# Optimization experiments

Measured on AMD Instinct MI355X. Metric: run time of the kernel, lower is better.

Reference implementation:

```python
import jax, jax.numpy as jnp
import numpy as np

N = 10000
E = 160000
IN_CH, HID, OUT = 14, 128, 4
HEADS = 8
NEG_SLOPE = 0.2


def setup_inputs() -> dict:
    key = jax.random.key(0)
    ks = jax.random.split(key, 16)
    glorot = lambda k, shape: jax.random.normal(k, shape, jnp.float32) * np.sqrt(2.0 / (shape[0] + shape[-1]))
    inp = {
        'x': jax.random.normal(ks[0], (N, IN_CH), jnp.float32),
        'edge_index': jax.random.randint(ks[1], (2, E), 0, N, jnp.int64),
        # layer 1: 14 -> 8 heads x 128, concat
        'W1': glorot(ks[2], (IN_CH, HEADS * HID)),
        'a_src1': glorot(ks[3], (HEADS, HID)),
        'a_dst1': glorot(ks[4], (HEADS, HID)),
        'b1': jnp.zeros((HEADS * HID,), jnp.float32),
        # layer 2: 1024 -> 8 heads x 128, concat
        'W2': glorot(ks[5], (HEADS * HID, HEADS * HID)),
        'a_src2': glorot(ks[6], (HEADS, HID)),
        'a_dst2': glorot(ks[7], (HEADS, HID)),
        'b2': jnp.zeros((HEADS * HID,), jnp.float32),
        # layer 3: 1024 -> 1 head x 4, mean (concat=False)
        'W3': glorot(ks[8], (HEADS * HID, OUT)),
        'a_src3': glorot(ks[9], (1, OUT)),
        'a_dst3': glorot(ks[10], (1, OUT)),
        'b3': jnp.zeros((OUT,), jnp.float32),
    }
    return inp


def gat_conv(x, src, dst, W, a_src, a_dst, b, heads, out_ch, concat):
    n = x.shape[0]
    h = (x @ W).reshape(n, heads, out_ch)                      # [N,H,C]
    al_s = jnp.sum(h * a_src, axis=-1)                         # [N,H]
    al_d = jnp.sum(h * a_dst, axis=-1)                         # [N,H]
    e = al_s[src] + al_d[dst]                                  # [E,H]
    e = jnp.where(e > 0, e, NEG_SLOPE * e)                     # LeakyReLU(0.2)
    # segment softmax over incoming edges of each dst node
    m = jax.ops.segment_max(e, dst, num_segments=n)
    ex = jnp.exp(e - m[dst])
    z = jax.ops.segment_sum(ex, dst, num_segments=n)
    alpha = ex / (z[dst] + 1e-16)                              # [E,H]
    out = jax.ops.segment_sum(h[src] * alpha[:, :, None], dst, num_segments=n)  # [N,H,C]
    out = out.reshape(n, heads * out_ch) if concat else out.mean(axis=1)
    return out + b


def reference(x, edge_index, W1, a_src1, a_dst1, b1, W2, a_src2, a_dst2, b2, W3, a_src3, a_dst3, b3):
    n = x.shape[0]
    # add self-loops (PyG GATConv default)
    loop = jnp.arange(n, dtype=edge_index.dtype)
    src = jnp.concatenate([edge_index[0], loop])
    dst = jnp.concatenate([edge_index[1], loop])
    # dropout layers are identity in eval mode
    h = gat_conv(x, src, dst, W1, a_src1, a_dst1, b1, HEADS, HID, True)
    h = jax.nn.relu(h)
    h = gat_conv(h, src, dst, W2, a_src2, a_dst2, b2, HEADS, HID, True)
    h = jax.nn.relu(h)
    h = gat_conv(h, src, dst, W3, a_src3, a_dst3, b3, 1, OUT, False)
    h = jax.nn.relu(h)
    return h
```

## Files before the change

### kernel.cpp

```cpp
#include <hip/hip_runtime.h>

typedef unsigned short ushort_t;
typedef unsigned int uint32;

#define N_NODES 10000
#define N_EDGES 160000
#define ET (N_NODES + N_EDGES)
#define MPAD 10112
#define HT 1024
#define HEADS 8
#define NEG 0.2f

#define O_FLAG     0
#define O_SRC      256
#define O_DST      (O_SRC + 680192)
#define O_COUNTS   (O_DST + 680192)
#define O_OFFS     (O_COUNTS + 40192)
#define O_CURS     (O_OFFS + 40192)
#define O_SSORT    (O_CURS + 40192)
#define O_ALS      (O_SSORT + 680192)
#define O_ALD      (O_ALS + 320000)
#define O_AL3S     (O_ALD + 320000)
#define O_AL3D     (O_AL3S + 40192)
#define O_H3       (O_AL3D + 40192)
#define O_XF       (O_H3 + 160000)
#define O_W1F      (O_XF + 560128)
#define O_AS1F     (O_W1F + 57344)
#define O_W3F      (O_AS1F + 24576)
#define O_S3F      (O_W3F + 16384)
#define O_W2T      (O_S3F + 768)
#define O_BUFA     (O_W2T + 2097152)
#define O_BUFB     (O_BUFA + 20709376)

__device__ __forceinline__ float bf2f(ushort_t u){ return __uint_as_float(((uint32)u) << 16); }
__device__ __forceinline__ ushort_t f2bf(float f){
    uint32 x = __float_as_uint(f);
    return (ushort_t)((x + 0x7fffu + ((x >> 16) & 1u)) >> 16);
}
__device__ __forceinline__ void unpack2(uint32 u, float& lo, float& hi){
    lo = __uint_as_float(u << 16);
    hi = __uint_as_float(u & 0xffff0000u);
}

typedef __bf16 bf16x8 __attribute__((ext_vector_type(8)));
typedef float  f32x4  __attribute__((ext_vector_type(4)));

typedef const __attribute__((address_space(1))) uint32* gas1_u32;
typedef       __attribute__((address_space(3))) uint32* las3_u32;

__device__ __forceinline__ void gload_lds16(const void* g, void* l){
    __builtin_amdgcn_global_load_lds((gas1_u32)g, (las3_u32)l, 16, 0, 0);
}

__device__ __forceinline__ int probe_f32(const uint32* __restrict__ w){
    int cnt = 0;
    for (int i = 0; i < 256; i++){
        uint32 e = (w[i] >> 7) & 0xffu;
        cnt += (e >= 64u && e <= 160u) ? 1 : 0;
    }
    return (cnt > 200) ? 0 : 1;
}
__device__ __forceinline__ int probe_edge64(const int* __restrict__ ei){
    int nz = 0;
    for (int i = 0; i < 128; i++) nz |= ei[2*i + 1];
    return (nz == 0) ? 1 : 0;
}

struct CvtArgs {
    const void* src[12];
    float*      dst[12];
    int         n[12];
};

__global__ __launch_bounds__(256) void k_setup(CvtArgs a, const void* __restrict__ W2,
                                               const uint32* __restrict__ w1raw,
                                               const int* __restrict__ eiraw,
                                               int* __restrict__ counts,
                                               ushort_t* __restrict__ W2T,
                                               int* __restrict__ flags){
    __shared__ ushort_t tile[32][33];
    int slice = blockIdx.y;
    int tid = threadIdx.x;
    if (slice < 12){
        int n = a.n[slice];
        int base = blockIdx.x * 1024 + tid * 4;
        if (base >= n) return;
        int f32 = probe_f32(w1raw);
        const void* s = a.src[slice];
        float* d = a.dst[slice];
        #pragma unroll
        for (int j = 0; j < 4; j++){
            int i = base + j;
            if (i < n) d[i] = f32 ? ((const float*)s)[i] : bf2f(((const ushort_t*)s)[i]);
        }
    } else if (slice == 12){
        if (blockIdx.x == 10){
            if (tid == 0) flags[0] = probe_edge64(eiraw);
            if (tid == 1) flags[1] = probe_f32(w1raw);
            return;
        }
        if (blockIdx.x < 10){
            int i0 = blockIdx.x * 1024 + tid * 4;
            if (i0 + 3 < N_NODES){
                *(int4*)(counts + i0) = make_int4(0,0,0,0);
            } else {
                for (int j = 0; j < 4; j++) if (i0 + j < N_NODES) counts[i0 + j] = 0;
            }
        }
    } else {
        int f32 = probe_f32(w1raw);
        int bx = blockIdx.x & 31, by = blockIdx.x >> 5;
        int cx = tid & 31;
        int ry = (tid >> 5) * 4;
        #pragma unroll
        for (int r = 0; r < 4; r++){
            size_t idx = (size_t)(by*32 + ry + r)*1024 + bx*32 + cx;
            tile[ry + r][cx] = f32 ? f2bf(((const float*)W2)[idx]) : ((const ushort_t*)W2)[idx];
        }
        __syncthreads();
        #pragma unroll
        for (int r = 0; r < 4; r++)
            W2T[(size_t)(bx*32 + ry + r)*1024 + by*32 + cx] = tile[cx][ry + r];
    }
}

__global__ __launch_bounds__(256) void k_extract_hist(const void* __restrict__ ei, const int* __restrict__ flags,
                                                      int* __restrict__ src, int* __restrict__ dst,
                                                      int* __restrict__ counts){
    int i = blockIdx.x * 256 + threadIdx.x;
    int is64 = flags[0];
    int s = -1, d = -1;
    if (i < N_EDGES){
        if (is64){
            const long long* p = (const long long*)ei;
            s = (int)p[i]; d = (int)p[N_EDGES + i];
        } else {
            const int* p = (const int*)ei;
            s = p[i]; d = p[N_EDGES + i];
        }
    } else if (i < ET){
        s = i - N_EDGES; d = s;
    }
    if (d >= 0){
        src[i] = s; dst[i] = d;
        atomicAdd(&counts[d], 1);
    }
}

__global__ __launch_bounds__(1024) void k_scan(const int* __restrict__ counts, int* __restrict__ offs,
                                               int* __restrict__ cursors, int n){
    __shared__ int wsum[16];
    __shared__ int running_s;
    int tid = threadIdx.x;
    int lane = tid & 63, wid = tid >> 6;
    if (tid == 0) running_s = 0;
    __syncthreads();
    for (int base = 0; base < n; base += 1024){
        int i = base + tid;
        int v = (i < n) ? counts[i] : 0;
        int x = v;
        #pragma unroll
        for (int d = 1; d < 64; d <<= 1){
            int t = __shfl_up(x, d, 64);
            if (lane >= d) x += t;
        }
        if (lane == 63) wsum[wid] = x;
        __syncthreads();
        if (wid == 0 && lane < 16){
            int w = wsum[lane];
            #pragma unroll
            for (int d = 1; d < 16; d <<= 1){
                int t = __shfl_up(w, d, 64);
                if (lane >= d) w += t;
            }
            wsum[lane] = w;
        }
        __syncthreads();
        int wprefix = (wid == 0) ? 0 : wsum[wid - 1];
        int run = running_s;
        int excl = run + wprefix + (x - v);
        if (i < n){ offs[i] = excl; cursors[i] = excl; }
        __syncthreads();
        if (tid == 0) running_s = run + wsum[15];
        __syncthreads();
    }
    if (tid == 0) offs[n] = running_s;
}

__global__ __launch_bounds__(256) void k_scatter(const int* __restrict__ src, const int* __restrict__ dst,
                                                 int* __restrict__ cursors, int* __restrict__ ssort){
    int i = blockIdx.x * 256 + threadIdx.x;
    if (i < ET){
        int pos = atomicAdd(&cursors[dst[i]], 1);
        ssort[pos] = src[i];
    }
}

__global__ __launch_bounds__(256) void k_gemm1f(const float* __restrict__ x, const float* __restrict__ W1,
                                                const float* __restrict__ a_src, const float* __restrict__ a_dst,
                                                ushort_t* __restrict__ h1,
                                                float* __restrict__ alS, float* __restrict__ alD){
    __shared__ float w1s[14 * HT];
    int tid = threadIdx.x;
    for (int i = tid * 4; i < 14 * HT; i += 1024)
        *(float4*)(w1s + i) = *(const float4*)(W1 + i);
    int c0 = tid * 4;
    float4 sv = *(const float4*)(a_src + c0);
    float4 dv = *(const float4*)(a_dst + c0);
    int head = tid >> 5, l32 = tid & 31;
    __syncthreads();
    for (int n = blockIdx.x; n < N_NODES; n += gridDim.x){
        float a0=0.f, a1=0.f, a2=0.f, a3=0.f;
        #pragma unroll
        for (int k = 0; k < 14; k++){
            float xv = x[n*14 + k];
            float4 w = *(const float4*)(w1s + k*HT + c0);
            a0 += xv*w.x; a1 += xv*w.y; a2 += xv*w.z; a3 += xv*w.w;
        }
        uint2 o;
        o.x = (uint32)f2bf(a0) | ((uint32)f2bf(a1) << 16);
        o.y = (uint32)f2bf(a2) | ((uint32)f2bf(a3) << 16);
        *(uint2*)(h1 + (size_t)n*HT + c0) = o;
        float h0,h1v,h2,h3v;
        unpack2(o.x, h0, h1v); unpack2(o.y, h2, h3v);
        float s = h0*sv.x + h1v*sv.y + h2*sv.z + h3v*sv.w;
        float d = h0*dv.x + h1v*dv.y + h2*dv.z + h3v*dv.w;
        #pragma unroll
        for (int of = 16; of; of >>= 1){ s += __shfl_xor(s, of, 32); d += __shfl_xor(d, of, 32); }
        if (l32 == 0){ alS[n*HEADS + head] = s; alD[n*HEADS + head] = d; }
    }
}

__global__ __launch_bounds__(256) void k_gat_agg(const ushort_t* __restrict__ H, const float* __restrict__ alS,
                                                 const float* __restrict__ alD, const int* __restrict__ offs,
                                                 const int* __restrict__ srcs, const float* __restrict__ bias,
                                                 ushort_t* __restrict__ out){
    int tid = threadIdx.x;
    int wv = tid >> 6, lane = tid & 63;
    int n = blockIdx.x * 2 + (wv >> 1);
    int half = wv & 1;
    int beg = offs[n], end = offs[n+1];
    int head = half*4 + (lane >> 4);
    float ad = alD[n*HEADS + head];

    int ch0 = half*512 + lane*8;
    const ushort_t* Hc = H + ch0;
    float m = -1e30f, z = 0.f;
    float c0=0.f,c1=0.f,c2=0.f,c3=0.f,c4=0.f,c5=0.f,c6=0.f,c7=0.f;
    for (int c = beg; c < end; c += 64){
        int cn = min(64, end - c);
        int sreg = (lane < cn) ? srcs[c + lane] : 0;
        int j = 0;
        for (; j + 4 <= cn; j += 4){
            int s0 = __shfl(sreg, j, 64);
            int s1 = __shfl(sreg, j+1, 64);
            int s2 = __shfl(sreg, j+2, 64);
            int s3 = __shfl(sreg, j+3, 64);
            uint4 u0 = *(const uint4*)(Hc + (size_t)s0*HT);
            uint4 u1 = *(const uint4*)(Hc + (size_t)s1*HT);
            uint4 u2 = *(const uint4*)(Hc + (size_t)s2*HT);
            uint4 u3 = *(const uint4*)(Hc + (size_t)s3*HT);
            float e0 = alS[s0*HEADS + head];
            float e1 = alS[s1*HEADS + head];
            float e2 = alS[s2*HEADS + head];
            float e3 = alS[s3*HEADS + head];
            float v0 = e0 + ad; v0 = v0 > 0.f ? v0 : NEG*v0;
            float v1 = e1 + ad; v1 = v1 > 0.f ? v1 : NEG*v1;
            float v2 = e2 + ad; v2 = v2 > 0.f ? v2 : NEG*v2;
            float v3 = e3 + ad; v3 = v3 > 0.f ? v3 : NEG*v3;
            float vm = fmaxf(fmaxf(v0, v1), fmaxf(v2, v3));
            if (vm > m){
                float sc = __expf(m - vm);
                z *= sc;
                c0*=sc; c1*=sc; c2*=sc; c3*=sc;
                c4*=sc; c5*=sc; c6*=sc; c7*=sc;
                m = vm;
            }
            float w0 = __expf(v0 - m);
            float w1 = __expf(v1 - m);
            float w2 = __expf(v2 - m);
            float w3 = __expf(v3 - m);
            z += (w0 + w1) + (w2 + w3);
            float f0,f1,f2,f3,f4,f5,f6,f7;
            unpack2(u0.x,f0,f1); unpack2(u0.y,f2,f3); unpack2(u0.z,f4,f5); unpack2(u0.w,f6,f7);
            c0+=w0*f0; c1+=w0*f1; c2+=w0*f2; c3+=w0*f3;
            c4+=w0*f4; c5+=w0*f5; c6+=w0*f6; c7+=w0*f7;
            unpack2(u1.x,f0,f1); unpack2(u1.y,f2,f3); unpack2(u1.z,f4,f5); unpack2(u1.w,f6,f7);
            c0+=w1*f0; c1+=w1*f1; c2+=w1*f2; c3+=w1*f3;
            c4+=w1*f4; c5+=w1*f5; c6+=w1*f6; c7+=w1*f7;
            unpack2(u2.x,f0,f1); unpack2(u2.y,f2,f3); unpack2(u2.z,f4,f5); unpack2(u2.w,f6,f7);
            c0+=w2*f0; c1+=w2*f1; c2+=w2*f2; c3+=w2*f3;
            c4+=w2*f4; c5+=w2*f5; c6+=w2*f6; c7+=w2*f7;
            unpack2(u3.x,f0,f1); unpack2(u3.y,f2,f3); unpack2(u3.z,f4,f5); unpack2(u3.w,f6,f7);
            c0+=w3*f0; c1+=w3*f1; c2+=w3*f2; c3+=w3*f3;
            c4+=w3*f4; c5+=w3*f5; c6+=w3*f6; c7+=w3*f7;
        }
        for (; j < cn; j++){
            int s0 = __shfl(sreg, j, 64);
            uint4 u0 = *(const uint4*)(Hc + (size_t)s0*HT);
            float v0 = alS[s0*HEADS + head] + ad;
            v0 = v0 > 0.f ? v0 : NEG*v0;
            if (v0 > m){
                float sc = __expf(m - v0);
                z *= sc;
                c0*=sc; c1*=sc; c2*=sc; c3*=sc;
                c4*=sc; c5*=sc; c6*=sc; c7*=sc;
                m = v0;
            }
            float w0 = __expf(v0 - m);
            z += w0;
            float f0,f1,f2,f3,f4,f5,f6,f7;
            unpack2(u0.x,f0,f1); unpack2(u0.y,f2,f3); unpack2(u0.z,f4,f5); unpack2(u0.w,f6,f7);
            c0+=w0*f0; c1+=w0*f1; c2+=w0*f2; c3+=w0*f3;
            c4+=w0*f4; c5+=w0*f5; c6+=w0*f6; c7+=w0*f7;
        }
    }
    float inv = 1.f / (z + 1e-16f);
    float4 b0 = *(const float4*)(bias + ch0);
    float4 b1 = *(const float4*)(bias + ch0 + 4);
    c0 = fmaxf(c0*inv+b0.x, 0.f); c1 = fmaxf(c1*inv+b0.y, 0.f);
    c2 = fmaxf(c2*inv+b0.z, 0.f); c3 = fmaxf(c3*inv+b0.w, 0.f);
    c4 = fmaxf(c4*inv+b1.x, 0.f); c5 = fmaxf(c5*inv+b1.y, 0.f);
    c6 = fmaxf(c6*inv+b1.z, 0.f); c7 = fmaxf(c7*inv+b1.w, 0.f);
    uint4 o;
    o.x = (uint32)f2bf(c0) | ((uint32)f2bf(c1) << 16);
    o.y = (uint32)f2bf(c2) | ((uint32)f2bf(c3) << 16);
    o.z = (uint32)f2bf(c4) | ((uint32)f2bf(c5) << 16);
    o.w = (uint32)f2bf(c6) | ((uint32)f2bf(c7) << 16);
    *(uint4*)(out + (size_t)n*HT + ch0) = o;
}

__global__ __launch_bounds__(256) void k_gemm2(const ushort_t* __restrict__ A, const ushort_t* __restrict__ BT,
                                               ushort_t* __restrict__ C,
                                               const float* __restrict__ aS, const float* __restrict__ aD,
                                               float* __restrict__ alS, float* __restrict__ alD){
    __shared__ ushort_t lbuf[2][2][128*64];
    float (*reds)[64][2] = (float (*)[64][2])lbuf;
    int L = blockIdx.x;
    int xcd = L & 7;
    int wi  = L >> 3;
    int bm  = xcd * 10 + (wi >> 3);
    int bn  = wi & 7;
    if (bm >= 79) return;
    int tid = threadIdx.x;
    int lane = tid & 63;
    int wave = tid >> 6;
    int wm = (wave & 1) * 64, wn = (wave >> 1) * 64;
    int lm = lane & 15, kg = lane >> 4;
    int c0 = (kg ^ (lm & 7)) * 8;
    f32x4 acc[4][4];
    #pragma unroll
    for (int i = 0; i < 4; i++)
        #pragma unroll
        for (int j = 0; j < 4; j++) acc[i][j] = (f32x4)0.0f;

    const int K = 1024;
    int rowA0 = bm * 128, rowB0 = bn * 128;

    auto stage = [&](int buf, int k0){
        #pragma unroll
        for (int it = 0; it < 4; ++it){
            int s = tid + it*256;
            int r = s >> 3;
            int q = (s & 7) ^ (r & 7);
            gload_lds16(A  + (size_t)(rowA0 + r)*K + k0 + q*8, &lbuf[buf][0][s*8]);
            gload_lds16(BT + (size_t)(rowB0 + r)*K + k0 + q*8, &lbuf[buf][1][s*8]);
        }
    };

    stage(0, 0);
    asm volatile("s_waitcnt vmcnt(0)" ::: "memory");
    __syncthreads();
    int cur = 0;
    for (int k0 = 0; k0 < K; k0 += 64){
        if (k0 + 64 < K) stage(cur ^ 1, k0 + 64);
        bf16x8 a0[4], a1[4], b0[4], b1[4];
        #pragma unroll
        for (int mt = 0; mt < 4; mt++){
            const ushort_t* base = &lbuf[cur][0][(wm + mt*16 + lm)*64];
            a0[mt] = *(const bf16x8*)(base + c0);
            a1[mt] = *(const bf16x8*)(base + (c0 ^ 32));
        }
        #pragma unroll
        for (int nt = 0; nt < 4; nt++){
            const ushort_t* base = &lbuf[cur][1][(wn + nt*16 + lm)*64];
            b0[nt] = *(const bf16x8*)(base + c0);
            b1[nt] = *(const bf16x8*)(base + (c0 ^ 32));
        }
        #pragma unroll
        for (int mt = 0; mt < 4; mt++)
            #pragma unroll
            for (int nt = 0; nt < 4; nt++)
                acc[mt][nt] = __builtin_amdgcn_mfma_f32_16x16x32_bf16(a0[mt], b0[nt], acc[mt][nt], 0, 0, 0);
        #pragma unroll
        for (int mt = 0; mt < 4; mt++)
            #pragma unroll
            for (int nt = 0; nt < 4; nt++)
                acc[mt][nt] = __builtin_amdgcn_mfma_f32_16x16x32_bf16(a1[mt], b1[nt], acc[mt][nt], 0, 0, 0);
        asm volatile("s_waitcnt vmcnt(0)" ::: "memory");
        __syncthreads();
        cur ^= 1;
    }
    #pragma unroll
    for (int mt = 0; mt < 4; mt++){
        int row_base = bm*128 + wm + mt*16 + kg*4;
        #pragma unroll
        for (int nt = 0; nt < 4; nt++){
            int col = bn*128 + wn + nt*16 + lm;
            #pragma unroll
            for (int r = 0; r < 4; r++){
                int row = row_base + r;
                if (row < N_NODES) C[(size_t)row*HT + col] = f2bf(acc[mt][nt][r]);
            }
        }
    }
    float as_l[4], ad_l[4];
    #pragma unroll
    for (int nt = 0; nt < 4; nt++){
        as_l[nt] = aS[bn*128 + wn + nt*16 + lm];
        ad_l[nt] = aD[bn*128 + wn + nt*16 + lm];
    }
    float psA[4][4], pdA[4][4];
    #pragma unroll
    for (int mt = 0; mt < 4; mt++){
        #pragma unroll
        for (int r = 0; r < 4; r++){
            float ps = acc[mt][0][r]*as_l[0] + acc[mt][1][r]*as_l[1]
                     + acc[mt][2][r]*as_l[2] + acc[mt][3][r]*as_l[3];
            float pd = acc[mt][0][r]*ad_l[0] + acc[mt][1][r]*ad_l[1]
                     + acc[mt][2][r]*ad_l[2] + acc[mt][3][r]*ad_l[3];
            #pragma unroll
            for (int o = 1; o < 16; o <<= 1){ ps += __shfl_xor(ps, o, 64); pd += __shfl_xor(pd, o, 64); }
            psA[mt][r] = ps; pdA[mt][r] = pd;
            if (wn == 64 && lm == 0){
                int rl = mt*16 + kg*4 + r;
                reds[wm >> 6][rl][0] = ps;
                reds[wm >> 6][rl][1] = pd;
            }
        }
    }
    __syncthreads();
    if (wn == 0 && lm == 0){
        #pragma unroll
        for (int mt = 0; mt < 4; mt++){
            #pragma unroll
            for (int r = 0; r < 4; r++){
                int rl = mt*16 + kg*4 + r;
                int row = bm*128 + wm + rl;
                if (row < N_NODES){
                    alS[row*HEADS + bn] = psA[mt][r] + reds[wm >> 6][rl][0];
                    alD[row*HEADS + bn] = pdA[mt][r] + reds[wm >> 6][rl][1];
                }
            }
        }
    }
}

__global__ __launch_bounds__(256) void k_gemm3(const ushort_t* __restrict__ A, const float* __restrict__ W3,
                                               const float* __restrict__ s3,
                                               float* __restrict__ h3, float* __restrict__ al3s, float* __restrict__ al3d){
    int tid = threadIdx.x;
    int lane = tid & 63, wave = tid >> 6;
    int n = blockIdx.x * 4 + wave;
    if (n >= N_NODES) return;
    float4 w3r[16];
    #pragma unroll
    for (int j = 0; j < 16; j++) w3r[j] = ((const float4*)W3)[lane*16 + j];
    const uint4* ap = (const uint4*)(A + (size_t)n*HT + lane*16);
    uint4 u0 = ap[0], u1 = ap[1];
    uint32 uu[8] = {u0.x,u0.y,u0.z,u0.w,u1.x,u1.y,u1.z,u1.w};
    float acc0=0.f, acc1=0.f, acc2=0.f, acc3=0.f;
    #pragma unroll
    for (int p = 0; p < 8; p++){
        float lo, hi;
        unpack2(uu[p], lo, hi);
        float4 wl = w3r[p*2], wh = w3r[p*2+1];
        acc0 += lo*wl.x + hi*wh.x;
        acc1 += lo*wl.y + hi*wh.y;
        acc2 += lo*wl.z + hi*wh.z;
        acc3 += lo*wl.w + hi*wh.w;
    }
    #pragma unroll
    for (int o = 32; o; o >>= 1){
        acc0 += __shfl_xor(acc0, o, 64); acc1 += __shfl_xor(acc1, o, 64);
        acc2 += __shfl_xor(acc2, o, 64); acc3 += __shfl_xor(acc3, o, 64);
    }
    if (lane == 0){
        *(float4*)(h3 + n*4) = make_float4(acc0, acc1, acc2, acc3);
        al3s[n] = acc0*s3[0] + acc1*s3[1] + acc2*s3[2] + acc3*s3[3];
        al3d[n] = acc0*s3[16] + acc1*s3[17] + acc2*s3[18] + acc3*s3[19];
    }
}

__global__ __launch_bounds__(256) void k_gat_agg3(const float* __restrict__ h3, const float* __restrict__ al3s,
                                                  const float* __restrict__ al3d, const int* __restrict__ offs,
                                                  const int* __restrict__ srcs, const float* __restrict__ b3,
                                                  const int* __restrict__ flags, void* __restrict__ out){
    int tid = threadIdx.x;
    int l = tid & 63, wave = tid >> 6;
    int n = blockIdx.x * 4 + wave;
    if (n >= N_NODES) return;
    int beg = offs[n], end = offs[n+1];
    float ad = al3d[n];
    float m = -1e30f;
    for (int e = beg + l; e < end; e += 64){
        float v = al3s[srcs[e]] + ad; v = v > 0.f ? v : NEG*v;
        m = fmaxf(m, v);
    }
    #pragma unroll
    for (int o = 32; o; o >>= 1) m = fmaxf(m, __shfl_xor(m, o, 64));
    float z = 0.f;
    for (int e = beg + l; e < end; e += 64){
        float v = al3s[srcs[e]] + ad; v = v > 0.f ? v : NEG*v;
        z += __expf(v - m);
    }
    #pragma unroll
    for (int o = 32; o; o >>= 1) z += __shfl_xor(z, o, 64);
    float inv = 1.f / (z + 1e-16f);
    float a0=0.f, a1=0.f, a2=0.f, a3=0.f;
    for (int e = beg + l; e < end; e += 64){
        int s = srcs[e];
        float v = al3s[s] + ad; v = v > 0.f ? v : NEG*v;
        float w = __expf(v - m) * inv;
        float4 hv = *(const float4*)(h3 + s*4);
        a0 += w*hv.x; a1 += w*hv.y; a2 += w*hv.z; a3 += w*hv.w;
    }
    #pragma unroll
    for (int o = 32; o; o >>= 1){
        a0 += __shfl_xor(a0, o, 64); a1 += __shfl_xor(a1, o, 64);
        a2 += __shfl_xor(a2, o, 64); a3 += __shfl_xor(a3, o, 64);
    }
    if (l == 0){
        float r0 = fmaxf(a0 + b3[0], 0.f);
        float r1 = fmaxf(a1 + b3[1], 0.f);
        float r2 = fmaxf(a2 + b3[2], 0.f);
        float r3 = fmaxf(a3 + b3[3], 0.f);
        if (flags[1]){
            float* o4 = (float*)out;
            o4[n*4+0]=r0; o4[n*4+1]=r1; o4[n*4+2]=r2; o4[n*4+3]=r3;
        } else {
            ushort_t* o2 = (ushort_t*)out;
            o2[n*4+0]=f2bf(r0); o2[n*4+1]=f2bf(r1); o2[n*4+2]=f2bf(r2); o2[n*4+3]=f2bf(r3);
        }
    }
}

extern "C" void kernel_launch(void* const* d_in, const int* in_sizes, int n_in,
                              void* d_out, int out_size, void* d_ws, size_t ws_size,
                              hipStream_t stream){
    const void* x   = d_in[0];
    const void* ei  = d_in[1];
    const void* W1  = d_in[2];
    const void* as1 = d_in[3];
    const void* ad1 = d_in[4];
    const void* b1  = d_in[5];
    const void* W2  = d_in[6];
    const void* as2 = d_in[7];
    const void* ad2 = d_in[8];
    const void* b2  = d_in[9];
    const void* W3  = d_in[10];
    const void* as3 = d_in[11];
    const void* ad3 = d_in[12];
    const void* b3  = d_in[13];

    char* ws = (char*)d_ws;
    int* flags     = (int*)(ws + O_FLAG);
    int* srcA      = (int*)(ws + O_SRC);
    int* dstA      = (int*)(ws + O_DST);
    int* counts    = (int*)(ws + O_COUNTS);
    int* offs      = (int*)(ws + O_OFFS);
    int* cursors   = (int*)(ws + O_CURS);
    int* ssort     = (int*)(ws + O_SSORT);
    float* alS     = (float*)(ws + O_ALS);
    float* alD     = (float*)(ws + O_ALD);
    float* al3s    = (float*)(ws + O_AL3S);
    float* al3d    = (float*)(ws + O_AL3D);
    float* h3      = (float*)(ws + O_H3);
    float* xF      = (float*)(ws + O_XF);
    float* W1F     = (float*)(ws + O_W1F);
    float* wvecF   = (float*)(ws + O_AS1F);
    float* W3F     = (float*)(ws + O_W3F);
    float* s3F     = (float*)(ws + O_S3F);
    ushort_t* W2T  = (ushort_t*)(ws + O_W2T);
    ushort_t* bufA = (ushort_t*)(ws + O_BUFA);
    ushort_t* bufB = (ushort_t*)(ws + O_BUFB);

    const int EB = (ET + 255) / 256;

    CvtArgs ca;
    ca.src[0]=x;   ca.dst[0]=xF;            ca.n[0]=140000;
    ca.src[1]=W1;  ca.dst[1]=W1F;           ca.n[1]=14336;
    ca.src[2]=as1; ca.dst[2]=wvecF+0*1024;  ca.n[2]=1024;
    ca.src[3]=ad1; ca.dst[3]=wvecF+1*1024;  ca.n[3]=1024;
    ca.src[4]=b1;  ca.dst[4]=wvecF+2*1024;  ca.n[4]=1024;
    ca.src[5]=as2; ca.dst[5]=wvecF+3*1024;  ca.n[5]=1024;
    ca.src[6]=ad2; ca.dst[6]=wvecF+4*1024;  ca.n[6]=1024;
    ca.src[7]=b2;  ca.dst[7]=wvecF+5*1024;  ca.n[7]=1024;
    ca.src[8]=W3;  ca.dst[8]=W3F;           ca.n[8]=4096;
    ca.src[9]=as3; ca.dst[9]=s3F+0;         ca.n[9]=4;
    ca.src[10]=ad3; ca.dst[10]=s3F+16;      ca.n[10]=4;
    ca.src[11]=b3;  ca.dst[11]=s3F+32;      ca.n[11]=4;

    k_setup<<<dim3(1024, 14), 256, 0, stream>>>(ca, W2, (const uint32*)W1, (const int*)ei,
                                                counts, W2T, flags);
    k_extract_hist<<<EB, 256, 0, stream>>>(ei, flags, srcA, dstA, counts);
    k_scan<<<1, 1024, 0, stream>>>(counts, offs, cursors, N_NODES);
    k_scatter<<<EB, 256, 0, stream>>>(srcA, dstA, cursors, ssort);

    k_gemm1f<<<512, 256, 0, stream>>>(xF, W1F, wvecF+0*1024, wvecF+1*1024, bufA, alS, alD);
    k_gat_agg<<<5000, 256, 0, stream>>>(bufA, alS, alD, offs, ssort, wvecF+2*1024, bufB);

    k_gemm2<<<640, 256, 0, stream>>>(bufB, W2T, bufA, wvecF+3*1024, wvecF+4*1024, alS, alD);
    k_gat_agg<<<5000, 256, 0, stream>>>(bufA, alS, alD, offs, ssort, wvecF+5*1024, bufB);

    k_gemm3<<<2500, 256, 0, stream>>>(bufB, W3F, s3F, h3, al3s, al3d);
    k_gat_agg3<<<2500, 256, 0, stream>>>(h3, al3s, al3d, offs, ssort, s3F+32, flags, d_out);
}
```

Measured before the change: 318.2 us.

## Restructure GAT aggregation: one wave per node-head, edge-parallel lane groups

The aggregation kernel now assigns each wave a single (node, head) pair. The four 16-lane groups in the wave process different edges in parallel, and their online-softmax partial states are merged at the end with cross-lane shuffles. The grid grows from 5000 to 20000 blocks, with the head index in the low block bits so neighbouring blocks share a node's source rows. The branchy max update is replaced by branchless FMA rescaling, and the output is written with a nontemporal store. This raises memory-level parallelism per node, but adds shuffle-reduction work and reads offsets and source lists once per head instead of once per node.

```diff
diff --git a/kernel.cpp b/kernel.cpp
--- a/kernel.cpp
+++ b/kernel.cpp
@@ -44,6 +44,7 @@
 
 typedef __bf16 bf16x8 __attribute__((ext_vector_type(8)));
 typedef float  f32x4  __attribute__((ext_vector_type(4)));
+typedef uint32 u32x4  __attribute__((ext_vector_type(4)));
 
 typedef const __attribute__((address_space(1))) uint32* gas1_u32;
 typedef       __attribute__((address_space(3))) uint32* las3_u32;
@@ -237,97 +238,104 @@
                                                  ushort_t* __restrict__ out){
     int tid = threadIdx.x;
     int wv = tid >> 6, lane = tid & 63;
-    int n = blockIdx.x * 2 + (wv >> 1);
-    int half = wv & 1;
+    int head = blockIdx.x & 7;
+    int n = (blockIdx.x >> 3) * 4 + wv;
+    if (n >= N_NODES) return;
     int beg = offs[n], end = offs[n+1];
-    int head = half*4 + (lane >> 4);
+    int g = lane >> 4;
+    int q = lane & 15;
     float ad = alD[n*HEADS + head];
-
-    int ch0 = half*512 + lane*8;
-    const ushort_t* Hc = H + ch0;
+    const ushort_t* Hh = H + head*128 + q*8;
+    const float NINF = -__int_as_float(0x7f800000);
+
     float m = -1e30f, z = 0.f;
     float c0=0.f,c1=0.f,c2=0.f,c3=0.f,c4=0.f,c5=0.f,c6=0.f,c7=0.f;
     for (int c = beg; c < end; c += 64){
         int cn = min(64, end - c);
         int sreg = (lane < cn) ? srcs[c + lane] : 0;
         int j = 0;
-        for (; j + 4 <= cn; j += 4){
-            int s0 = __shfl(sreg, j, 64);
-            int s1 = __shfl(sreg, j+1, 64);
-            int s2 = __shfl(sreg, j+2, 64);
-            int s3 = __shfl(sreg, j+3, 64);
-            uint4 u0 = *(const uint4*)(Hc + (size_t)s0*HT);
-            uint4 u1 = *(const uint4*)(Hc + (size_t)s1*HT);
-            uint4 u2 = *(const uint4*)(Hc + (size_t)s2*HT);
-            uint4 u3 = *(const uint4*)(Hc + (size_t)s3*HT);
-            float e0 = alS[s0*HEADS + head];
-            float e1 = alS[s1*HEADS + head];
-            float e2 = alS[s2*HEADS + head];
-            float e3 = alS[s3*HEADS + head];
-            float v0 = e0 + ad; v0 = v0 > 0.f ? v0 : NEG*v0;
-            float v1 = e1 + ad; v1 = v1 > 0.f ? v1 : NEG*v1;
-            float v2 = e2 + ad; v2 = v2 > 0.f ? v2 : NEG*v2;
-            float v3 = e3 + ad; v3 = v3 > 0.f ? v3 : NEG*v3;
-            float vm = fmaxf(fmaxf(v0, v1), fmaxf(v2, v3));
-            if (vm > m){
-                float sc = __expf(m - vm);
-                z *= sc;
-                c0*=sc; c1*=sc; c2*=sc; c3*=sc;
-                c4*=sc; c5*=sc; c6*=sc; c7*=sc;
-                m = vm;
-            }
-            float w0 = __expf(v0 - m);
-            float w1 = __expf(v1 - m);
-            float w2 = __expf(v2 - m);
-            float w3 = __expf(v3 - m);
-            z += (w0 + w1) + (w2 + w3);
+        for (; j + 8 <= cn; j += 8){
+            int s0 = __shfl(sreg, j + g, 64);
+            int s1 = __shfl(sreg, j + 4 + g, 64);
+            uint4 u0 = *(const uint4*)(Hh + (size_t)s0*HT);
+            uint4 u1 = *(const uint4*)(Hh + (size_t)s1*HT);
+            float v0 = alS[s0*HEADS + head] + ad; v0 = v0 > 0.f ? v0 : NEG*v0;
+            float v1 = alS[s1*HEADS + head] + ad; v1 = v1 > 0.f ? v1 : NEG*v1;
+            float nm = fmaxf(fmaxf(m, v0), v1);
+            float sc = __expf(m - nm);
+            float w0 = __expf(v0 - nm);
+            float w1 = __expf(v1 - nm);
+            m = nm;
+            z = z*sc + (w0 + w1);
+            float f0,f1,f2,f3,f4,f5,f6,f7;
+            float g0,g1,g2,g3,g4,g5,g6,g7;
+            unpack2(u0.x,f0,f1); unpack2(u0.y,f2,f3); unpack2(u0.z,f4,f5); unpack2(u0.w,f6,f7);
+            unpack2(u1.x,g0,g1); unpack2(u1.y,g2,g3); unpack2(u1.z,g4,g5); unpack2(u1.w,g6,g7);
+            c0 = fmaf(w1,g0, fmaf(w0,f0, c0*sc));
+            c1 = fmaf(w1,g1, fmaf(w0,f1, c1*sc));
+            c2 = fmaf(w1,g2, fmaf(w0,f2, c2*sc));
+            c3 = fmaf(w1,g3, fmaf(w0,f3, c3*sc));
+            c4 = fmaf(w1,g4, fmaf(w0,f4, c4*sc));
+            c5 = fmaf(w1,g5, fmaf(w0,f5, c5*sc));
+            c6 = fmaf(w1,g6, fmaf(w0,f6, c6*sc));
+            c7 = fmaf(w1,g7, fmaf(w0,f7, c7*sc));
+        }
+        for (; j < cn; j += 4){
+            int e = j + g;
+            int s0 = __shfl(sreg, e, 64);
+            uint4 u0 = *(const uint4*)(Hh + (size_t)s0*HT);
+            float v0 = alS[s0*HEADS + head] + ad; v0 = v0 > 0.f ? v0 : NEG*v0;
+            v0 = (e < cn) ? v0 : NINF;
+            float nm = fmaxf(m, v0);
+            float sc = __expf(m - nm);
+            float w0 = __expf(v0 - nm);
+            m = nm;
+            z = z*sc + w0;
             float f0,f1,f2,f3,f4,f5,f6,f7;
             unpack2(u0.x,f0,f1); unpack2(u0.y,f2,f3); unpack2(u0.z,f4,f5); unpack2(u0.w,f6,f7);
-            c0+=w0*f0; c1+=w0*f1; c2+=w0*f2; c3+=w0*f3;
-            c4+=w0*f4; c5+=w0*f5; c6+=w0*f6; c7+=w0*f7;
-            unpack2(u1.x,f0,f1); unpack2(u1.y,f2,f3); unpack2(u1.z,f4,f5); unpack2(u1.w,f6,f7);
-            c0+=w1*f0; c1+=w1*f1; c2+=w1*f2; c3+=w1*f3;
-            c4+=w1*f4; c5+=w1*f5; c6+=w1*f6; c7+=w1*f7;
-            unpack2(u2.x,f0,f1); unpack2(u2.y,f2,f3); unpack2(u2.z,f4,f5); unpack2(u2.w,f6,f7);
-            c0+=w2*f0; c1+=w2*f1; c2+=w2*f2; c3+=w2*f3;
-            c4+=w2*f4; c5+=w2*f5; c6+=w2*f6; c7+=w2*f7;
-            unpack2(u3.x,f0,f1); unpack2(u3.y,f2,f3); unpack2(u3.z,f4,f5); unpack2(u3.w,f6,f7);
-            c0+=w3*f0; c1+=w3*f1; c2+=w3*f2; c3+=w3*f3;
-            c4+=w3*f4; c5+=w3*f5; c6+=w3*f6; c7+=w3*f7;
-        }
-        for (; j < cn; j++){
-            int s0 = __shfl(sreg, j, 64);
-            uint4 u0 = *(const uint4*)(Hc + (size_t)s0*HT);
-            float v0 = alS[s0*HEADS + head] + ad;
-            v0 = v0 > 0.f ? v0 : NEG*v0;
-            if (v0 > m){
-                float sc = __expf(m - v0);
-                z *= sc;
-                c0*=sc; c1*=sc; c2*=sc; c3*=sc;
-                c4*=sc; c5*=sc; c6*=sc; c7*=sc;
-                m = v0;
-            }
-            float w0 = __expf(v0 - m);
-            z += w0;
-            float f0,f1,f2,f3,f4,f5,f6,f7;
-            unpack2(u0.x,f0,f1); unpack2(u0.y,f2,f3); unpack2(u0.z,f4,f5); unpack2(u0.w,f6,f7);
-            c0+=w0*f0; c1+=w0*f1; c2+=w0*f2; c3+=w0*f3;
-            c4+=w0*f4; c5+=w0*f5; c6+=w0*f6; c7+=w0*f7;
-        }
-    }
-    float inv = 1.f / (z + 1e-16f);
-    float4 b0 = *(const float4*)(bias + ch0);
-    float4 b1 = *(const float4*)(bias + ch0 + 4);
-    c0 = fmaxf(c0*inv+b0.x, 0.f); c1 = fmaxf(c1*inv+b0.y, 0.f);
-    c2 = fmaxf(c2*inv+b0.z, 0.f); c3 = fmaxf(c3*inv+b0.w, 0.f);
-    c4 = fmaxf(c4*inv+b1.x, 0.f); c5 = fmaxf(c5*inv+b1.y, 0.f);
-    c6 = fmaxf(c6*inv+b1.z, 0.f); c7 = fmaxf(c7*inv+b1.w, 0.f);
-    uint4 o;
-    o.x = (uint32)f2bf(c0) | ((uint32)f2bf(c1) << 16);
-    o.y = (uint32)f2bf(c2) | ((uint32)f2bf(c3) << 16);
-    o.z = (uint32)f2bf(c4) | ((uint32)f2bf(c5) << 16);
-    o.w = (uint32)f2bf(c6) | ((uint32)f2bf(c7) << 16);
-    *(uint4*)(out + (size_t)n*HT + ch0) = o;
+            c0 = fmaf(w0,f0, c0*sc); c1 = fmaf(w0,f1, c1*sc);
+            c2 = fmaf(w0,f2, c2*sc); c3 = fmaf(w0,f3, c3*sc);
+            c4 = fmaf(w0,f4, c4*sc); c5 = fmaf(w0,f5, c5*sc);
+            c6 = fmaf(w0,f6, c6*sc); c7 = fmaf(w0,f7, c7*sc);
+        }
+    }
+    #pragma unroll
+    for (int off = 16; off < 64; off <<= 1){
+        float m2 = __shfl_xor(m, off, 64);
+        float z2 = __shfl_xor(z, off, 64);
+        float d0 = __shfl_xor(c0, off, 64);
+        float d1 = __shfl_xor(c1, off, 64);
+        float d2 = __shfl_xor(c2, off, 64);
+        float d3 = __shfl_xor(c3, off, 64);
+        float d4 = __shfl_xor(c4, off, 64);
+        float d5 = __shfl_xor(c5, off, 64);
+        float d6 = __shfl_xor(c6, off, 64);
+        float d7 = __shfl_xor(c7, off, 64);
+        float nm = fmaxf(m, m2);
+        float a = __expf(m - nm), b = __expf(m2 - nm);
+        z = z*a + z2*b;
+        c0 = c0*a + d0*b; c1 = c1*a + d1*b;
+        c2 = c2*a + d2*b; c3 = c3*a + d3*b;
+        c4 = c4*a + d4*b; c5 = c5*a + d5*b;
+        c6 = c6*a + d6*b; c7 = c7*a + d7*b;
+        m = nm;
+    }
+    if (g == 0){
+        float inv = 1.f / (z + 1e-16f);
+        int ch0 = head*128 + q*8;
+        float4 b0 = *(const float4*)(bias + ch0);
+        float4 b1 = *(const float4*)(bias + ch0 + 4);
+        c0 = fmaxf(c0*inv+b0.x, 0.f); c1 = fmaxf(c1*inv+b0.y, 0.f);
+        c2 = fmaxf(c2*inv+b0.z, 0.f); c3 = fmaxf(c3*inv+b0.w, 0.f);
+        c4 = fmaxf(c4*inv+b1.x, 0.f); c5 = fmaxf(c5*inv+b1.y, 0.f);
+        c6 = fmaxf(c6*inv+b1.z, 0.f); c7 = fmaxf(c7*inv+b1.w, 0.f);
+        u32x4 o;
+        o.x = (uint32)f2bf(c0) | ((uint32)f2bf(c1) << 16);
+        o.y = (uint32)f2bf(c2) | ((uint32)f2bf(c3) << 16);
+        o.z = (uint32)f2bf(c4) | ((uint32)f2bf(c5) << 16);
+        o.w = (uint32)f2bf(c6) | ((uint32)f2bf(c7) << 16);
+        __builtin_nontemporal_store(o, (u32x4*)(out + (size_t)n*HT + ch0));
+    }
 }
 
 __global__ __launch_bounds__(256) void k_gemm2(const ushort_t* __restrict__ A, const ushort_t* __restrict__ BT,
@@ -608,10 +616,10 @@
     k_scatter<<<EB, 256, 0, stream>>>(srcA, dstA, cursors, ssort);
 
     k_gemm1f<<<512, 256, 0, stream>>>(xF, W1F, wvecF+0*1024, wvecF+1*1024, bufA, alS, alD);
-    k_gat_agg<<<5000, 256, 0, stream>>>(bufA, alS, alD, offs, ssort, wvecF+2*1024, bufB);
+    k_gat_agg<<<20000, 256, 0, stream>>>(bufA, alS, alD, offs, ssort, wvecF+2*1024, bufB);
 
     k_gemm2<<<640, 256, 0, stream>>>(bufB, W2T, bufA, wvecF+3*1024, wvecF+4*1024, alS, alD);
-    k_gat_agg<<<5000, 256, 0, stream>>>(bufA, alS, alD, offs, ssort, wvecF+5*1024, bufB);
+    k_gat_agg<<<20000, 256, 0, stream>>>(bufA, alS, alD, offs, ssort, wvecF+5*1024, bufB);
 
     k_gemm3<<<2500, 256, 0, stream>>>(bufB, W3F, s3F, h3, al3s, al3d);
     k_gat_agg3<<<2500, 256, 0, stream>>>(h3, al3s, al3d, offs, ssort, s3F+32, flags, d_out);
```

Result: no change. 321.4 us (+1.0%).
